# Kernel optimization log

Measured on AMD Instinct MI355X. Metric: run time of the kernel, lower is better.

Reference implementation:

```python
import jax, jax.numpy as jnp
import numpy as np

H = 16        # query heads
D = 4         # KV downsampling -> H//D = 4 kv heads
WINDOW = 1024 # sliding window
THETA = 10000.0


def _rope_cos_sin(L, dim):
    freqs = 1.0 / (THETA ** (jnp.arange(0, dim - 1, 2, dtype=jnp.float32) / dim))
    ang = jnp.arange(L, dtype=jnp.float32)[:, None] * freqs[None, :]  # (L, dim//2)
    return jnp.cos(ang), jnp.sin(ang)


def _apply_rope(x, cos, sin):
    # x: (N, h, L, dim); interleaved complex pairs (even=real, odd=imag)
    xr, xi = x[..., 0::2], x[..., 1::2]
    orr = xr * cos - xi * sin
    oii = xr * sin + xi * cos
    return jnp.stack([orr, oii], axis=-1).reshape(x.shape)


def setup_inputs() -> dict:
    key = jax.random.key(0)
    ks = jax.random.split(key, 5)
    N, L, E = 4, 2048, 2048
    return {
        "x": jax.random.normal(ks[0], (N, L, E), dtype=jnp.float32),
        "Wq": jax.random.normal(ks[1], (E, E), dtype=jnp.float32) * 0.02,
        "Wk": jax.random.normal(ks[2], (E // D, E), dtype=jnp.float32) * 0.02,
        "Wv": jax.random.normal(ks[3], (E // D, E), dtype=jnp.float32) * 0.02,
        "Wo": jax.random.normal(ks[4], (E, E), dtype=jnp.float32) * 0.02,
    }


def reference(x, Wq, Wk, Wv, Wo):
    N, L, E = x.shape
    dim = E // H  # 128 per-head dim (same for q and downsampled k/v)
    Hkv = H // D

    q = (x @ Wq.T).reshape(N, L, H, dim).transpose(0, 2, 1, 3)      # (N,H,L,d)
    k = (x @ Wk.T).reshape(N, L, Hkv, dim).transpose(0, 2, 1, 3)    # (N,Hkv,L,d)
    v = (x @ Wv.T).reshape(N, L, Hkv, dim).transpose(0, 2, 1, 3)

    cos, sin = _rope_cos_sin(L, dim)
    q = _apply_rope(q, cos, sin)
    k = _apply_rope(k, cos, sin)

    # GQA: expand kv heads (repeat_interleave along head axis)
    k = jnp.repeat(k, D, axis=1)  # (N,H,L,d)
    v = jnp.repeat(v, D, axis=1)

    scale = 1.0 / jnp.sqrt(jnp.float32(dim))
    attn = jnp.einsum("bhld,bhsd->bhls", q, k) * scale  # (N,H,L,L)

    i = jnp.arange(L)[:, None]
    j = jnp.arange(L)[None, :]
    allowed = (j <= i) & (j > i - WINDOW)  # causal + sliding window
    attn = jnp.where(allowed[None, None], attn, -jnp.inf)
    attn = jax.nn.softmax(attn, axis=-1)

    z = jnp.einsum("bhls,bhsd->bhld", attn, v)  # (N,H,L,d)
    z = z.transpose(0, 2, 1, 3).reshape(N, L, E)
    return z @ Wo.T
```

## Files before the change

kernel.cpp:

```cpp
#include <hip/hip_runtime.h>
#include <hip/hip_bf16.h>
#include <math.h>

typedef unsigned short u16;
typedef unsigned int u32;
typedef __attribute__((ext_vector_type(8))) short short8;
typedef __attribute__((ext_vector_type(8))) u16 ushort8;
typedef __attribute__((ext_vector_type(4))) float f32x4;
typedef __attribute__((ext_vector_type(16))) float f32x16;
typedef __attribute__((ext_vector_type(4))) u32 u32x4;

#define N_B 4
#define L_S 2048
#define E_D 2048
#define NH 16
#define HD 128
#define WIN 1024
#define QW 3072
#define LOG2E 1.4426950408889634f

static __device__ __forceinline__ u16 f32_bf16(float f) {
  u32 u = __builtin_bit_cast(u32, f);
  u = (u + 0x7fffu + ((u >> 16) & 1u)) >> 16;
  return (u16)u;
}
static __device__ __forceinline__ float bf16_f32(u16 h) {
  u32 u = ((u32)h) << 16;
  return __builtin_bit_cast(float, u);
}
static __device__ __forceinline__ u32 pack_bf16_pair(float lo, float hi) {
  __hip_bfloat162 h2 = __float22bfloat162_rn(make_float2(lo, hi));
  u32 r;
  __builtin_memcpy(&r, &h2, 4);
  return r;
}
static __device__ __forceinline__ void gload_lds16(const void* g, void* l) {
  __builtin_amdgcn_global_load_lds((__attribute__((address_space(1))) void*)g,
                                   (__attribute__((address_space(3))) void*)l, 16, 0, 0);
}

__global__ void k_cast(const float* __restrict__ src, u16* __restrict__ dst, int n8) {
  int i = blockIdx.x * blockDim.x + threadIdx.x;
  if (i >= n8) return;
  const float4* s = (const float4*)src + (size_t)i * 2;
  float4 a = s[0], b = s[1];
  ushort8 v;
  v[0] = f32_bf16(a.x); v[1] = f32_bf16(a.y); v[2] = f32_bf16(a.z); v[3] = f32_bf16(a.w);
  v[4] = f32_bf16(b.x); v[5] = f32_bf16(b.y); v[6] = f32_bf16(b.z); v[7] = f32_bf16(b.w);
  *((ushort8*)dst + i) = v;
}

__global__ void k_rope_table(float* __restrict__ cs, float* __restrict__ sn) {
  int idx = blockIdx.x * blockDim.x + threadIdx.x;
  int l = idx >> 6, f = idx & 63;
  float freq = exp2f(-(float)f * (13.287712379549449f / 64.0f));
  float ang = (float)l * freq;
  cs[idx] = cosf(ang);
  sn[idx] = sinf(ang);
}

__global__ void k_rope_apply(u16* __restrict__ QKV, const float* __restrict__ cs,
                             const float* __restrict__ sn) {
  int idx = blockIdx.x * blockDim.x + threadIdx.x;
  int f = idx & 63;
  int rest = idx >> 6;
  int hh = rest % 20;
  int row = rest / 20;
  int l = row & (L_S - 1);
  int col = (hh < NH) ? (hh * HD + 2 * f) : (E_D + (hh - NH) * HD + 2 * f);
  u32* p = (u32*)(QKV + (size_t)row * QW + col);
  u32 v = *p;
  float xr = bf16_f32((u16)(v & 0xffffu));
  float xi = bf16_f32((u16)(v >> 16));
  float c = cs[l * 64 + f], s = sn[l * 64 + f];
  float orr = xr * c - xi * s;
  float oii = xr * s + xi * c;
  *p = (u32)f32_bf16(orr) | ((u32)f32_bf16(oii) << 16);
}

template <int OUT_F32>
__global__ __launch_bounds__(512, 1) void k_gemm256(
    const u16* __restrict__ A, int lda,
    const u16* __restrict__ B, int ldb,
    void* __restrict__ Cp, int ldc, int K) {
  __shared__ __align__(16) u16 Ab[3 * 8192];
  __shared__ __align__(16) u16 Bb[3 * 8192];
  const int tid = threadIdx.x;
  const int lane = tid & 63, w = tid >> 6;
  const int lr = lane & 15, lg = lane >> 4;
  const int wm = w >> 2, wn = w & 3;
  const int fid = blockIdx.x;
  const int cc = fid & 7, l = fid >> 3;
  const int m0 = (cc * 4 + (l & 3)) * 256;
  const int n0 = (l >> 2) * 256;
  const int rswz = (lr & 6) << 3;

  auto STAGE = [&](int kt, int bb) {
    const int r2 = tid >> 2;
    const int ce = (((tid & 3) * 16) ^ ((r2 & 6) << 3)) >> 1;
#pragma unroll
    for (int rr = 0; rr < 2; ++rr) {
      int row = rr * 128 + r2;
      gload_lds16(A + (size_t)(m0 + row) * lda + kt * 32 + ce,
                  (char*)Ab + bb * 16384 + rr * 8192 + (w << 10));
      gload_lds16(B + (size_t)(n0 + row) * ldb + kt * 32 + ce,
                  (char*)Bb + bb * 16384 + rr * 8192 + (w << 10));
    }
  };

  f32x4 acc[8][4];
  const f32x4 z4 = {0.f, 0.f, 0.f, 0.f};
#pragma unroll
  for (int mf = 0; mf < 8; ++mf)
#pragma unroll
    for (int nf = 0; nf < 4; ++nf) acc[mf][nf] = z4;

  const int nt = K >> 5;
  STAGE(0, 0);
  STAGE(1, 1);
  asm volatile("s_waitcnt vmcnt(4)" ::: "memory");
  __builtin_amdgcn_sched_barrier(0);
  __builtin_amdgcn_s_barrier();
  __builtin_amdgcn_sched_barrier(0);

  int c3 = 0;
  for (int t = 0; t < nt; ++t) {
    int ib = c3 + 2; if (ib >= 3) ib -= 3;
    if (t + 2 < nt) STAGE(t + 2, ib);
    const char* Abt = (const char*)Ab + c3 * 16384;
    const char* Bbt = (const char*)Bb + c3 * 16384;
    short8 af[8], bf[4];
#pragma unroll
    for (int nf = 0; nf < 4; ++nf) {
      int row = wn * 64 + nf * 16 + lr;
      bf[nf] = *(const short8*)(Bbt + row * 64 + ((lg * 16) ^ rswz));
    }
#pragma unroll
    for (int mf = 0; mf < 8; ++mf) {
      int row = wm * 128 + mf * 16 + lr;
      af[mf] = *(const short8*)(Abt + row * 64 + ((lg * 16) ^ rswz));
    }
    __builtin_amdgcn_s_setprio(1);
#pragma unroll
    for (int mf = 0; mf < 8; ++mf)
#pragma unroll
      for (int nf = 0; nf < 4; ++nf)
        acc[mf][nf] =
            __builtin_amdgcn_mfma_f32_16x16x32_bf16(af[mf], bf[nf], acc[mf][nf], 0, 0, 0);
    __builtin_amdgcn_s_setprio(0);
    if (t + 2 < nt)
      asm volatile("s_waitcnt vmcnt(4) lgkmcnt(0)" ::: "memory");
    else
      asm volatile("s_waitcnt vmcnt(0) lgkmcnt(0)" ::: "memory");
    __builtin_amdgcn_sched_barrier(0);
    __builtin_amdgcn_s_barrier();
    __builtin_amdgcn_sched_barrier(0);
    c3 = (c3 == 2) ? 0 : c3 + 1;
  }

#pragma unroll
  for (int mf = 0; mf < 8; ++mf)
#pragma unroll
    for (int nf = 0; nf < 4; ++nf)
#pragma unroll
      for (int j = 0; j < 4; ++j) {
        size_t r = (size_t)(m0 + wm * 128 + mf * 16 + lg * 4 + j);
        int c = n0 + wn * 64 + nf * 16 + lr;
        if (OUT_F32)
          ((float*)Cp)[r * ldc + c] = acc[mf][nf][j];
        else
          ((u16*)Cp)[r * ldc + c] = f32_bf16(acc[mf][nf][j]);
      }
}

__global__ __launch_bounds__(512, 2) void k_attn(u16* __restrict__ QKV) {
  const int bx = blockIdx.x, h = blockIdx.y, b = blockIdx.z;
  const int qb = (b >= 2) ? 7 - bx : bx;
  const int tid = threadIdx.x;
  const int lane = tid & 63, w = tid >> 6;
  const int l31 = lane & 31, hi = lane >> 5;
  const int kh = h >> 2;
  const int qs = qb * 256 + w * 32;
  __shared__ __align__(16) u16 Klds[2][64 * 128];
  __shared__ __align__(16) u16 Vt[2][128 * 64];
  const float SCL2 = 0.08838834764831845f * 1.4426950408889634f;
  const size_t bL = (size_t)b * L_S;
  const int q = qs + l31;
  const size_t rowQ = (bL + q) * QW + h * HD;
  short8 qf[8];
#pragma unroll
  for (int ds = 0; ds < 8; ++ds)
    qf[ds] = *(const short8*)(QKV + rowQ + ds * 16 + hi * 8);
  f32x16 o[4];
#pragma unroll
  for (int dt = 0; dt < 4; ++dt)
#pragma unroll
    for (int r = 0; r < 16; ++r) o[dt][r] = 0.f;
  float m2 = -3e38f, lsum = 0.f;
  int t0 = qb * 256 - (WIN - 1);
  if (t0 < 0) t0 = 0;
  t0 >>= 6;
  const int t1 = 4 * qb + 3;
  short8 vreg[2];

  auto ISSUE_K = [&](int t, int buf) {
    char* Kb = (char*)Klds + buf * 16384;
#pragma unroll
    for (int rr = 0; rr < 2; ++rr) {
      int row = rr * 32 + (tid >> 4);
      int colb = ((tid & 15) * 16) ^ ((row & 7) << 4);
      gload_lds16(QKV + (bL + t * 64 + row) * QW + E_D + kh * HD + (colb >> 1),
                  Kb + rr * 8192 + w * 1024 + (lane << 4));
    }
  };
  auto LOAD_V = [&](int t) {
#pragma unroll
    for (int rr = 0; rr < 2; ++rr)
      vreg[rr] = *(const short8*)(QKV + (bL + t * 64 + lane) * QW + E_D + 512 + kh * HD +
                                  ((w * 2 + rr) * 8));
  };
  auto WRITE_V = [&](int buf) {
    char* Vb = (char*)Vt + buf * 16384;
#pragma unroll
    for (int rr = 0; rr < 2; ++rr) {
      int db = (w * 2 + rr) * 8;
#pragma unroll
      for (int e = 0; e < 8; ++e)
        *(u16*)(Vb + ((((db + e) * 128) + lane * 2) ^ (e << 4))) = (u16)vreg[rr][e];
    }
  };

  LOAD_V(t0);
  ISSUE_K(t0, 0);
  __syncthreads();
  WRITE_V(0);
  int c = 0;

  for (int t = t0; t <= t1; ++t) {
    const int kv0 = t * 64;
    const int tn = (t < t1) ? t + 1 : t1;
    ISSUE_K(tn, c ^ 1);
    LOAD_V(tn);
    const bool act = (kv0 <= qs + 31) && (kv0 + 63 > qs - WIN);
    u32x4 pa[4];
    if (act) {
      char* Kb = (char*)Klds + c * 16384;
      f32x16 s[2];
#pragma unroll
      for (int g = 0; g < 2; ++g)
#pragma unroll
        for (int r = 0; r < 16; ++r) s[g][r] = 0.f;
#pragma unroll
      for (int g = 0; g < 2; ++g) {
        const int r = g * 32 + l31;
        const int rsw = (r & 7) << 4;
#pragma unroll
        for (int ds = 0; ds < 8; ++ds) {
          short8 kf = *(const short8*)(Kb + (r * 256 + ((ds * 32 + hi * 16) ^ rsw)));
          s[g] = __builtin_amdgcn_mfma_f32_32x32x16_bf16(kf, qf[ds], s[g], 0, 0, 0);
        }
      }
      float v[2][16];
      float mx = -3e38f;
#pragma unroll
      for (int g = 0; g < 2; ++g)
#pragma unroll
        for (int r = 0; r < 16; ++r) {
          int kg = kv0 + g * 32 + (r & 3) + 8 * (r >> 2) + 4 * hi;
          bool a = (kg <= q) && (kg > q - WIN);
          float vv = a ? s[g][r] * SCL2 : -3e38f;
          v[g][r] = vv;
          mx = fmaxf(mx, vv);
        }
      mx = fmaxf(mx, __shfl_xor(mx, 32));
      if (__ballot(mx > m2 + 11.5415603f)) {
        float mn = fmaxf(m2, mx);
        float alpha = exp2f(m2 - mn);
        m2 = mn;
        lsum *= alpha;
#pragma unroll
        for (int r = 0; r < 16; ++r) {
          float alr = __shfl(alpha, (r & 3) + 8 * (r >> 2) + 4 * hi);
#pragma unroll
          for (int dt = 0; dt < 4; ++dt) o[dt][r] *= alr;
        }
      }
      float rs = 0.f;
#pragma unroll
      for (int g = 0; g < 2; ++g)
#pragma unroll
        for (int r = 0; r < 16; ++r) {
          float pe = (v[g][r] > -1e37f) ? exp2f(v[g][r] - m2) : 0.f;
          v[g][r] = pe;
          rs += pe;
        }
      rs += __shfl_xor(rs, 32);
      lsum += rs;
#pragma unroll
      for (int g = 0; g < 2; ++g) {
        u32 W[8];
#pragma unroll
        for (int qi = 0; qi < 4; ++qi) {
          W[2 * qi]     = pack_bf16_pair(v[g][4 * qi + 0], v[g][4 * qi + 1]);
          W[2 * qi + 1] = pack_bf16_pair(v[g][4 * qi + 2], v[g][4 * qi + 3]);
        }
        u32 R[4];
        R[0] = __shfl_xor(hi ? W[0] : W[2], 32);
        R[1] = __shfl_xor(hi ? W[1] : W[3], 32);
        R[2] = __shfl_xor(hi ? W[4] : W[6], 32);
        R[3] = __shfl_xor(hi ? W[5] : W[7], 32);
#pragma unroll
        for (int ksl = 0; ksl < 2; ++ksl) {
          u32x4 fr;
          if (hi == 0) {
            fr[0] = W[4 * ksl]; fr[1] = W[4 * ksl + 1];
            fr[2] = R[2 * ksl]; fr[3] = R[2 * ksl + 1];
          } else {
            fr[0] = R[2 * ksl]; fr[1] = R[2 * ksl + 1];
            fr[2] = W[4 * ksl + 2]; fr[3] = W[4 * ksl + 3];
          }
          pa[g * 2 + ksl] = fr;
        }
      }
    }
    __syncthreads();
    WRITE_V(c ^ 1);
    if (act) {
      char* Vb = (char*)Vt + c * 16384;
      __builtin_amdgcn_s_setprio(1);
#pragma unroll
      for (int dt = 0; dt < 4; ++dt) {
        const int d = dt * 32 + l31;
        const int dsw = (d & 7) << 4;
#pragma unroll
        for (int ks = 0; ks < 4; ++ks) {
          short8 vf = *(const short8*)(Vb + (d * 128 + ((ks * 32 + hi * 16) ^ dsw)));
          o[dt] = __builtin_amdgcn_mfma_f32_32x32x16_bf16(
              __builtin_bit_cast(short8, pa[ks]), vf, o[dt], 0, 0, 0);
        }
      }
      __builtin_amdgcn_s_setprio(0);
    }
    c ^= 1;
  }
  float inv = 1.0f / lsum;
#pragma unroll
  for (int r = 0; r < 16; ++r) {
    int ridx = (r & 3) + 8 * (r >> 2) + 4 * hi;
    float invr = __shfl(inv, ridx);
    size_t rowO = (bL + qs + ridx) * QW + h * HD + l31;
#pragma unroll
    for (int dt = 0; dt < 4; ++dt)
      QKV[rowO + dt * 32] = f32_bf16(o[dt][r] * invr);
  }
}

extern "C" void kernel_launch(void* const* d_in, const int* in_sizes, int n_in,
                              void* d_out, int out_size, void* d_ws, size_t ws_size,
                              hipStream_t stream) {
  const float* x  = (const float*)d_in[0];
  const float* Wq = (const float*)d_in[1];
  const float* Wk = (const float*)d_in[2];
  const float* Wv = (const float*)d_in[3];
  const float* Wo = (const float*)d_in[4];
  char* ws = (char*)d_ws;
  if (ws_size < 105906176u) return;
  u16* xb    = (u16*)(ws);
  u16* Wqkv  = (u16*)(ws + 33554432);
  u16* Wob   = (u16*)(ws + 46137344);
  u16* QKV   = (u16*)(ws + 54525952);
  float* cs  = (float*)(ws + 104857600);
  float* sn  = (float*)(ws + 105381888);

  k_cast<<<8192, 256, 0, stream>>>(x, xb, 16777216 / 8);
  k_cast<<<2048, 256, 0, stream>>>(Wq, Wqkv, 4194304 / 8);
  k_cast<<<512, 256, 0, stream>>>(Wk, Wqkv + 2048 * 2048, 1048576 / 8);
  k_cast<<<512, 256, 0, stream>>>(Wv, Wqkv + 2560 * 2048, 1048576 / 8);
  k_cast<<<2048, 256, 0, stream>>>(Wo, Wob, 4194304 / 8);
  k_rope_table<<<512, 256, 0, stream>>>(cs, sn);
  k_gemm256<0><<<384, 512, 0, stream>>>(xb, 2048, Wqkv, 2048, QKV, QW, 2048);
  k_rope_apply<<<40960, 256, 0, stream>>>(QKV, cs, sn);
  k_attn<<<dim3(8, 16, 4), 512, 0, stream>>>(QKV);
  k_gemm256<1><<<256, 512, 0, stream>>>(QKV, QW, Wob, 2048, d_out, 2048, 2048);
}
```

Baseline: 427.3 us.

## Restructure GEMM into 8-phase pipeline with K=64 tiles and interleaved staging

Replaces the triple-buffered K=32 GEMM mainloop with a double-buffered K=64 tile, split into four sub-phases per tile (two M halves times two K halves). Global-to-LDS loads for the next tiles are interleaved between the MFMA phases, and the LDS swizzle key changes. The aim is to overlap memory traffic with MFMA work more finely and to halve the outer loop trip count. The cost is more barriers per tile and a more intricate staging order, which could stall if the wait counts are mis-tuned.

```diff
diff --git a/kernel.cpp b/kernel.cpp
--- a/kernel.cpp
+++ b/kernel.cpp
@@ -79,12 +79,12 @@
 }
 
 template <int OUT_F32>
-__global__ __launch_bounds__(512, 1) void k_gemm256(
+__global__ __launch_bounds__(512, 1) void k_gemm8p(
     const u16* __restrict__ A, int lda,
     const u16* __restrict__ B, int ldb,
     void* __restrict__ Cp, int ldc, int K) {
-  __shared__ __align__(16) u16 Ab[3 * 8192];
-  __shared__ __align__(16) u16 Bb[3 * 8192];
+  __shared__ __align__(16) char Ab[2][4][8192];
+  __shared__ __align__(16) char Bb[2][2][16384];
   const int tid = threadIdx.x;
   const int lane = tid & 63, w = tid >> 6;
   const int lr = lane & 15, lg = lane >> 4;
@@ -93,19 +93,23 @@
   const int cc = fid & 7, l = fid >> 3;
   const int m0 = (cc * 4 + (l & 3)) * 256;
   const int n0 = (l >> 2) * 256;
-  const int rswz = (lr & 6) << 3;
-
-  auto STAGE = [&](int kt, int bb) {
-    const int r2 = tid >> 2;
-    const int ce = (((tid & 3) * 16) ^ ((r2 & 6) << 3)) >> 1;
-#pragma unroll
-    for (int rr = 0; rr < 2; ++rr) {
-      int row = rr * 128 + r2;
-      gload_lds16(A + (size_t)(m0 + row) * lda + kt * 32 + ce,
-                  (char*)Ab + bb * 16384 + rr * 8192 + (w << 10));
-      gload_lds16(B + (size_t)(n0 + row) * ldb + kt * 32 + ce,
-                  (char*)Bb + bb * 16384 + rr * 8192 + (w << 10));
-    }
+  const int nt = K >> 6;
+  const int srow = tid >> 2;
+  const int skey = (srow & 3) << 4;
+  const int scolb = ((tid & 3) * 16) ^ skey;
+  const int rkey = (lr & 3) << 4;
+
+  auto STAGE_A = [&](int T, int qm, int kk) {
+    if (T >= nt) return;
+    int g = m0 + qm * 64 + (srow & 63) + (srow >> 6) * 128;
+    gload_lds16(A + (size_t)g * lda + T * 64 + kk * 32 + (scolb >> 1),
+                &Ab[T & 1][qm * 2 + kk][0] + (tid << 4));
+  };
+  auto STAGE_B = [&](int T, int kk, int h) {
+    if (T >= nt) return;
+    int g = n0 + h * 128 + srow;
+    gload_lds16(B + (size_t)g * ldb + T * 64 + kk * 32 + (scolb >> 1),
+                &Bb[T & 1][kk][0] + h * 8192 + (tid << 4));
   };
 
   f32x4 acc[8][4];
@@ -115,47 +119,52 @@
 #pragma unroll
     for (int nf = 0; nf < 4; ++nf) acc[mf][nf] = z4;
 
-  const int nt = K >> 5;
-  STAGE(0, 0);
-  STAGE(1, 1);
-  asm volatile("s_waitcnt vmcnt(4)" ::: "memory");
+#pragma unroll
+  for (int T = 0; T < 2; ++T) {
+    STAGE_A(T, 0, 0); STAGE_A(T, 0, 1); STAGE_A(T, 1, 0); STAGE_A(T, 1, 1);
+    STAGE_B(T, 0, 0); STAGE_B(T, 0, 1); STAGE_B(T, 1, 0); STAGE_B(T, 1, 1);
+  }
+  asm volatile("s_waitcnt vmcnt(8)" ::: "memory");
   __builtin_amdgcn_sched_barrier(0);
   __builtin_amdgcn_s_barrier();
   __builtin_amdgcn_sched_barrier(0);
 
-  int c3 = 0;
   for (int t = 0; t < nt; ++t) {
-    int ib = c3 + 2; if (ib >= 3) ib -= 3;
-    if (t + 2 < nt) STAGE(t + 2, ib);
-    const char* Abt = (const char*)Ab + c3 * 16384;
-    const char* Bbt = (const char*)Bb + c3 * 16384;
-    short8 af[8], bf[4];
-#pragma unroll
-    for (int nf = 0; nf < 4; ++nf) {
-      int row = wn * 64 + nf * 16 + lr;
-      bf[nf] = *(const short8*)(Bbt + row * 64 + ((lg * 16) ^ rswz));
-    }
-#pragma unroll
-    for (int mf = 0; mf < 8; ++mf) {
-      int row = wm * 128 + mf * 16 + lr;
-      af[mf] = *(const short8*)(Abt + row * 64 + ((lg * 16) ^ rswz));
-    }
-    __builtin_amdgcn_s_setprio(1);
-#pragma unroll
-    for (int mf = 0; mf < 8; ++mf)
-#pragma unroll
-      for (int nf = 0; nf < 4; ++nf)
-        acc[mf][nf] =
-            __builtin_amdgcn_mfma_f32_16x16x32_bf16(af[mf], bf[nf], acc[mf][nf], 0, 0, 0);
-    __builtin_amdgcn_s_setprio(0);
-    if (t + 2 < nt)
-      asm volatile("s_waitcnt vmcnt(4) lgkmcnt(0)" ::: "memory");
-    else
-      asm volatile("s_waitcnt vmcnt(0) lgkmcnt(0)" ::: "memory");
-    __builtin_amdgcn_sched_barrier(0);
-    __builtin_amdgcn_s_barrier();
-    __builtin_amdgcn_sched_barrier(0);
-    c3 = (c3 == 2) ? 0 : c3 + 1;
+    const int s = t & 1;
+#pragma unroll
+    for (int p = 0; p < 4; ++p) {
+      const int qm = p & 1, kk = p >> 1;
+      if (p == 0)      { STAGE_A(t + 1, 1, 1); STAGE_B(t + 1, 1, 0); }
+      else if (p == 1) { STAGE_B(t + 1, 1, 1); STAGE_A(t + 2, 0, 0); }
+      else if (p == 2) { STAGE_A(t + 2, 1, 0); STAGE_B(t + 2, 0, 0); }
+      else             { STAGE_B(t + 2, 0, 1); STAGE_A(t + 2, 0, 1); }
+      short8 af[4], bf[4];
+#pragma unroll
+      for (int mf = 0; mf < 4; ++mf) {
+        int row = wm * 64 + mf * 16 + lr;
+        af[mf] = *(const short8*)(&Ab[s][qm * 2 + kk][0] + row * 64 + ((lg * 16) ^ rkey));
+      }
+#pragma unroll
+      for (int nf = 0; nf < 4; ++nf) {
+        int row = wn * 64 + nf * 16 + lr;
+        bf[nf] = *(const short8*)(&Bb[s][kk][0] + row * 64 + ((lg * 16) ^ rkey));
+      }
+      if (p == 3)
+        asm volatile("s_waitcnt vmcnt(4) lgkmcnt(0)" ::: "memory");
+      else
+        asm volatile("s_waitcnt lgkmcnt(0)" ::: "memory");
+      __builtin_amdgcn_sched_barrier(0);
+      __builtin_amdgcn_s_barrier();
+      __builtin_amdgcn_sched_barrier(0);
+      __builtin_amdgcn_s_setprio(1);
+#pragma unroll
+      for (int mf = 0; mf < 4; ++mf)
+#pragma unroll
+        for (int nf = 0; nf < 4; ++nf)
+          acc[qm * 4 + mf][nf] =
+              __builtin_amdgcn_mfma_f32_16x16x32_bf16(af[mf], bf[nf], acc[qm * 4 + mf][nf], 0, 0, 0);
+      __builtin_amdgcn_s_setprio(0);
+    }
   }
 
 #pragma unroll
@@ -378,8 +387,8 @@
   k_cast<<<512, 256, 0, stream>>>(Wv, Wqkv + 2560 * 2048, 1048576 / 8);
   k_cast<<<2048, 256, 0, stream>>>(Wo, Wob, 4194304 / 8);
   k_rope_table<<<512, 256, 0, stream>>>(cs, sn);
-  k_gemm256<0><<<384, 512, 0, stream>>>(xb, 2048, Wqkv, 2048, QKV, QW, 2048);
+  k_gemm8p<0><<<384, 512, 0, stream>>>(xb, 2048, Wqkv, 2048, QKV, QW, 2048);
   k_rope_apply<<<40960, 256, 0, stream>>>(QKV, cs, sn);
   k_attn<<<dim3(8, 16, 4), 512, 0, stream>>>(QKV);
-  k_gemm256<1><<<256, 512, 0, stream>>>(QKV, QW, Wob, 2048, d_out, 2048, 2048);
-}
+  k_gemm8p<1><<<256, 512, 0, stream>>>(QKV, QW, Wob, 2048, d_out, 2048, 2048);
+}
```

New measurement: 477.9 us. 11.8% more time.
